# Kernel optimization log

Measured on AMD Instinct MI355X. Metric: run time of the kernel, lower is better.

The kernel has to match this reference:

```python
import jax, jax.numpy as jnp
from jax import lax
import numpy as np

B, L, IN_DIM, HID, BINS = 1, 384, 41, 64, 63
ATTN_DIM, NUM_ANCHORS = 32, 32
NUM_CONV, ATTN_EVERY = 6, 2
SIGMA, EPS = 12.0, 1e-5
DILATIONS = [1, 2, 4, 8, 16]


def select_anchors(length, k):
    # deterministic 'stride' mode of select_anchors
    k = max(1, min(k, length))
    stride = max(1, length // k)
    idx = np.arange(0, length, stride)[:k]
    if idx.size < k:
        idx = np.concatenate([idx, np.full(k - idx.size, length - 1)])
    return jnp.asarray(idx, dtype=jnp.int32)


def conv2d(x, w, b, dilation=1):
    # x: (b, Cin, H, W), w: (Cout, Cin, kh, kw) -- 'same' padding like torch padding=dilation*(k//2)
    pad = dilation * (w.shape[-1] // 2)
    y = lax.conv_general_dilated(x, w, (1, 1), [(pad, pad), (pad, pad)],
                                 rhs_dilation=(dilation, dilation),
                                 dimension_numbers=('NCHW', 'OIHW', 'NCHW'))
    return y + b[None, :, None, None]


def instance_norm(x):
    # torch InstanceNorm2d(affine=False), eps=1e-5, per (b, c) over spatial dims
    mu = x.mean(axis=(2, 3), keepdims=True)
    var = x.var(axis=(2, 3), keepdims=True)
    return (x - mu) * lax.rsqrt(var + EPS)


def anchor_attention(pair, td, tq, anchors, wq, wl, wr, wvl, wvr, wo, wg, bg,
                     tg_w1, tg_b1, tg_w2, tg_b2):
    # pair: (b, L, L, d); td: (b, L, L); tq: (b,)
    q = pair @ wq                                    # (b, L, L, a)
    p_left = pair[:, :, anchors, :]                  # (b, L, K, d)
    p_right = pair[:, anchors, :, :]                 # (b, K, L, d)
    left = p_left @ wl                               # (b, L, K, a)
    right = p_right @ wr                             # (b, K, L, a)
    scores = jnp.einsum('bija,bika->bijk', q, left)
    scores = scores + jnp.einsum('bija,bkja->bijk', q, right)
    scores = scores / jnp.sqrt(jnp.float32(ATTN_DIM))
    # template bias, 'consistency' mode
    t_left = td[:, :, anchors]                       # (b, L, K)
    t_right = jnp.swapaxes(td[:, anchors, :], 1, 2)  # (b, L, K)
    t_sum = t_left[:, :, None, :] + t_right[:, None, :, :]  # (b, L, L, K)
    bias = -jnp.abs(t_sum - td[..., None]) / SIGMA
    # TemplateGate
    coverage = (td > 0).astype(jnp.float32).mean(axis=(1, 2))        # (b,)
    length_norm = jnp.full_like(coverage, td.shape[-1] / 512.0)
    feats = jnp.stack([coverage, tq, length_norm], axis=-1)          # (b, 3)
    g = jax.nn.sigmoid(jax.nn.relu(feats @ tg_w1 + tg_b1) @ tg_w2 + tg_b2)  # (b, 1)
    scores = scores + g[:, :, None, None] * bias
    attn = jax.nn.softmax(scores, axis=-1)
    v_left = p_left @ wvl                            # (b, L, K, a)
    v_right = p_right @ wvr                          # (b, K, L, a)
    update = jnp.einsum('bijk,bika->bija', attn, v_left)
    update = update + jnp.einsum('bijk,bkja->bija', attn, v_right)
    update = update @ wo                             # (b, L, L, d)
    gate = jax.nn.sigmoid(pair @ wg + bg)
    return pair + gate * update


def setup_inputs() -> dict:
    key = jax.random.key(0)
    ks = iter(jax.random.split(key, 40))

    def rn(shape, scale=0.05):
        return jax.random.normal(next(ks), shape, dtype=jnp.float32) * scale

    return dict(
        features=jax.random.normal(next(ks), (B, L, L, IN_DIM), dtype=jnp.float32),
        template_dist=jax.random.uniform(next(ks), (B, L, L), dtype=jnp.float32) * 20.0,
        template_quality=jax.random.uniform(next(ks), (B,), dtype=jnp.float32),
        in_w=rn((HID, IN_DIM, 1, 1)), in_b=rn((HID,)),
        conv1_w=rn((NUM_CONV, HID, HID, 3, 3)), conv1_b=rn((NUM_CONV, HID)),
        conv2_w=rn((NUM_CONV, HID, HID, 3, 3)), conv2_b=rn((NUM_CONV, HID)),
        wq=rn((HID, ATTN_DIM)), wl=rn((HID, ATTN_DIM)), wr=rn((HID, ATTN_DIM)),
        wvl=rn((HID, ATTN_DIM)), wvr=rn((HID, ATTN_DIM)), wo=rn((ATTN_DIM, HID)),
        wg=rn((HID, HID)), bg=rn((HID,)),
        tg_w1=rn((3, 16)), tg_b1=rn((16,)), tg_w2=rn((16, 1)), tg_b2=rn((1,)),
        dist_w=rn((BINS, HID, 3, 3)), dist_b=rn((BINS,)),
        cf_w1=rn((32, BINS, 3, 3)), cf_b1=rn((32,)),
        cf_w2=rn((32, 32, 3, 3)), cf_b2=rn((32,)),
        cf_w3=rn((1, 32, 1, 1)), cf_b3=rn((1,)),
    )


def reference(features, template_dist, template_quality, in_w, in_b,
              conv1_w, conv1_b, conv2_w, conv2_b,
              wq, wl, wr, wvl, wvr, wo, wg, bg, tg_w1, tg_b1, tg_w2, tg_b2,
              dist_w, dist_b, cf_w1, cf_b1, cf_w2, cf_b2, cf_w3, cf_b3):
    anchors = select_anchors(L, NUM_ANCHORS)
    x = conv2d(jnp.transpose(features, (0, 3, 1, 2)), in_w, in_b)  # (b, hid, L, L)
    num_attn = max(1, NUM_CONV // max(1, ATTN_EVERY))
    attn_added = 0
    for i in range(NUM_CONV):
        d = DILATIONS[i % len(DILATIONS)]
        res = x
        out = jax.nn.elu(instance_norm(conv2d(x, conv1_w[i], conv1_b[i], d)))
        out = instance_norm(conv2d(out, conv2_w[i], conv2_b[i], 1))
        x = jax.nn.elu(out + res)
        if (i + 1) % ATTN_EVERY == 0 and attn_added < num_attn:
            pair = jnp.transpose(x, (0, 2, 3, 1))
            pair = anchor_attention(pair, template_dist, template_quality, anchors,
                                    wq, wl, wr, wvl, wvr, wo, wg, bg,
                                    tg_w1, tg_b1, tg_w2, tg_b2)
            x = jnp.transpose(pair, (0, 3, 1, 2))
            attn_added += 1
    logits = conv2d(x, dist_w, dist_b)                       # (b, bins, L, L)
    logits = 0.5 * (logits + jnp.swapaxes(logits, 2, 3))     # symmetrize_pairs
    c = jax.nn.relu(conv2d(logits, cf_w1, cf_b1))
    c = jax.nn.relu(conv2d(c, cf_w2, cf_b2))
    confidence = jax.nn.sigmoid(conv2d(c, cf_w3, cf_b3))[:, 0]   # (b, L, L)
    distance_logits = jnp.transpose(logits, (0, 2, 3, 1))        # (b, L, L, bins)
    return distance_logits, confidence
```

## Files before the change

kernel.cpp:

```cpp
#include <hip/hip_runtime.h>
#include <math.h>

#define LDIM 384
#define NPIX (LDIM*LDIM)
#define NBINS 63

typedef __attribute__((ext_vector_type(8))) __bf16 bf16x8;
typedef __attribute__((ext_vector_type(4))) float floatx4;

__device__ __forceinline__ float sigf(float x){ return 1.f/(1.f+expf(-x)); }

__global__ __launch_bounds__(256) void prep_kernel(
    const float* __restrict__ c1w, const float* __restrict__ c2w,
    const float* __restrict__ dw, const float* __restrict__ cf1w,
    const float* __restrict__ cf2w, const float* __restrict__ wg,
    const float* __restrict__ wo, const float* __restrict__ wq,
    __bf16* __restrict__ Wf){
  int idx = blockIdx.x*256 + threadIdx.x;
  if (idx >= 515072) return;
  if (idx >= 506880){
    int rel, NT, NDIM; const float* src;
    if (idx < 510976){ rel = idx - 506880; src = wg; NT=4; NDIM=64; }
    else if (idx < 513024){ rel = idx - 510976; src = wo; NT=4; NDIM=64; }
    else { rel = idx - 513024; src = wq; NT=2; NDIM=32; }
    int j = rel & 7, lane = (rel>>3) & 63;
    int r2 = rel >> 9;
    int nt = r2 % NT, kc = r2 / NT;
    int k = kc*32 + (lane>>4)*8 + j;
    int n = nt*16 + (lane&15);
    Wf[idx] = (__bf16)src[(size_t)k*NDIM + n];
    return;
  }
  const float* src; int ICreal, OCreal, ICP, NT, rel;
  if (idx < 442368){
    int layer = idx / 36864; rel = idx - layer*36864;
    int i = layer >> 1;
    src = (layer & 1) ? (c2w + (size_t)i*36864) : (c1w + (size_t)i*36864);
    ICreal=64; OCreal=64; ICP=64; NT=4;
  } else if (idx < 479232){
    rel = idx - 442368; src = dw;   ICreal=64; OCreal=63; ICP=64; NT=4;
  } else if (idx < 497664){
    rel = idx - 479232; src = cf1w; ICreal=63; OCreal=32; ICP=64; NT=2;
  } else {
    rel = idx - 497664; src = cf2w; ICreal=32; OCreal=32; ICP=32; NT=2;
  }
  int j = rel & 7, lane = (rel>>3) & 63;
  int r2 = rel >> 9;
  int nt = r2 % NT; int r3 = r2 / NT;
  int KC = ICP/32;
  int kc = r3 % KC; int tap = r3 / KC;
  int k = kc*32 + (lane>>4)*8 + j;
  int n = nt*16 + (lane&15);
  float v = 0.f;
  if (k < ICreal && n < OCreal) v = src[((size_t)n*ICreal + k)*9 + tap];
  Wf[idx] = (__bf16)v;
}

template<int ICP, int NT, int D, int WAVES>
__global__ __launch_bounds__(WAVES*64) void mfma_conv(
    const __bf16* __restrict__ Ain, const __bf16* __restrict__ Wf,
    const float* __restrict__ bias, int OC_real,
    float* __restrict__ outF, __bf16* __restrict__ outP,
    int relu, float* __restrict__ ostats){
  constexpr int KC = ICP/32;
  constexpr int OCS = NT*16;
  constexpr int REC_B = ICP*4;
  __shared__ float red[OCS*WAVES*2];
  const int t = threadIdx.x;
  const int wave = t>>6, lane = t&63;
  const int q = lane>>4, col16 = lane&15;
  const int y = blockIdx.y;
  const int x0 = blockIdx.x*(WAVES*16);
  const int gx0 = x0 + wave*16 + col16;

  floatx4 acc[NT];
  #pragma unroll
  for (int b=0;b<NT;b++){ floatx4 z = {0.f,0.f,0.f,0.f}; acc[b]=z; }

  #pragma unroll
  for (int ky=0; ky<3; ky++){
    const int yr = y + (ky-1)*D;
    if ((unsigned)yr < LDIM){
      const char* rowb = (const char*)Ain + (size_t)yr*LDIM*REC_B + q*16;
      #pragma unroll
      for (int kx=0; kx<3; kx++){
        const int gx = gx0 + (kx-1)*D;
        bf16x8 ah[KC], al[KC];
        #pragma unroll
        for (int kc=0;kc<KC;kc++){
          #pragma unroll
          for (int j=0;j<8;j++){ ah[kc][j]=(__bf16)0.f; al[kc][j]=(__bf16)0.f; }
        }
        if ((unsigned)gx < LDIM){
          const char* p = rowb + (size_t)gx*REC_B;
          #pragma unroll
          for (int kc=0;kc<KC;kc++){
            ah[kc] = *(const bf16x8*)(p + kc*64);
            al[kc] = *(const bf16x8*)(p + kc*64 + ICP*2);
          }
        }
        #pragma unroll
        for (int kc=0;kc<KC;kc++){
          const __bf16* wkc = Wf + (size_t)((ky*3+kx)*KC + kc)*NT*512 + lane*8;
          #pragma unroll
          for (int nt=0; nt<NT; nt++){
            bf16x8 bfrag = *(const bf16x8*)(wkc + (size_t)nt*512);
            acc[nt] = __builtin_amdgcn_mfma_f32_16x16x32_bf16(ah[kc], bfrag, acc[nt], 0,0,0);
            acc[nt] = __builtin_amdgcn_mfma_f32_16x16x32_bf16(al[kc], bfrag, acc[nt], 0,0,0);
          }
        }
      }
    }
  }

  #pragma unroll
  for (int nt=0; nt<NT; nt++){
    int oc = nt*16 + col16;
    float bv = (oc < OC_real) ? bias[oc] : 0.f;
    int pxb = x0 + wave*16 + q*4;
    float s=0.f, sq=0.f;
    #pragma unroll
    for (int r=0; r<4; r++){
      float vv = acc[nt][r] + bv;
      if (relu) vv = fmaxf(vv, 0.f);
      size_t pix = (size_t)y*LDIM + pxb + r;
      if (outF) outF[pix*OCS + oc] = vv;
      if (outP){
        __bf16 h = (__bf16)vv;
        __bf16* rec = outP + pix*(size_t)(OCS*2);
        rec[oc] = h; rec[OCS+oc] = (__bf16)(vv - (float)h);
      }
      s += vv; sq += vv*vv;
    }
    if (ostats){
      s  += __shfl_xor(s, 16);  s  += __shfl_xor(s, 32);
      sq += __shfl_xor(sq, 16); sq += __shfl_xor(sq, 32);
      if (q == 0){
        red[oc*WAVES + wave] = s;
        red[OCS*WAVES + oc*WAVES + wave] = sq;
      }
    }
  }
  if (ostats){
    __syncthreads();
    float* oslot = ostats + ((blockIdx.y & 7) << 7);
    if (t < OCS){
      float s=0.f, sq=0.f;
      #pragma unroll
      for (int w=0; w<WAVES; w++){
        s  += red[t*WAVES + w];
        sq += red[OCS*WAVES + t*WAVES + w];
      }
      atomicAdd(&oslot[t], s);
      atomicAdd(&oslot[64+t], sq);
    }
  }
}

__global__ __launch_bounds__(256) void in_proj_kernel(
    const float* __restrict__ feat, const float* __restrict__ w,
    const float* __restrict__ b, __bf16* __restrict__ PX){
  __shared__ float sf[16][41];
  __shared__ float sw[64*41];
  int t = threadIdx.x;
  size_t p0 = (size_t)blockIdx.x*16;
  float wv[11];
  #pragma unroll
  for (int k=0;k<11;k++){ int idx=t+k*256; wv[k] = (idx<2624) ? w[idx] : 0.f; }
  float fv[3];
  #pragma unroll
  for (int k=0;k<3;k++){ int idx=t+k*256; fv[k] = (idx<656) ? feat[p0*41 + idx] : 0.f; }
  #pragma unroll
  for (int k=0;k<11;k++){ int idx=t+k*256; if (idx<2624) sw[idx]=wv[k]; }
  #pragma unroll
  for (int k=0;k<3;k++){
    int idx=t+k*256;
    if (idx<656){ int p = idx/41, k2 = idx - p*41; sf[p][k2]=fv[k]; }
  }
  __syncthreads();
  #pragma unroll
  for (int k=0;k<4;k++){
    int item = t + k*256;
    int c = item&63, p = item>>6;
    float acc = b[c];
    #pragma unroll
    for (int kk=0;kk<41;kk++) acc += sf[p][kk]*sw[c*41+kk];
    __bf16 h = (__bf16)acc;
    __bf16* rec = PX + (p0+p)*128;
    rec[c] = h; rec[64+c] = (__bf16)(acc - (float)h);
  }
}

__global__ __launch_bounds__(256) void norm_elu_planes(
    __bf16* __restrict__ U, const float* __restrict__ stats){
  size_t idx = (size_t)blockIdx.x*256 + threadIdx.x;
  size_t px = idx>>3; int c0 = (int)(idx&7)*8;
  __bf16* ur = U + px*128;
  uint4 uh = *(const uint4*)(ur + c0);
  uint4 ul = *(const uint4*)(ur + 64 + c0);
  __bf16* uhp=(__bf16*)&uh; __bf16* ulp=(__bf16*)&ul;
  float mu[8], rs[8];
  #pragma unroll
  for (int k=0;k<8;k++){
    int c = c0+k;
    float s=0.f, sq=0.f;
    #pragma unroll
    for (int rp=0;rp<8;rp++){ s += stats[rp*128 + c]; sq += stats[rp*128 + 64 + c]; }
    float m = s*(1.f/NPIX);
    mu[k]=m; rs[k]=rsqrtf(sq*(1.f/NPIX) - m*m + 1e-5f);
  }
  #pragma unroll
  for (int k=0;k<8;k++){
    float v = ((float)uhp[k] + (float)ulp[k] - mu[k])*rs[k];
    v = v>0.f ? v : expm1f(v);
    __bf16 h = (__bf16)v; uhp[k]=h; ulp[k]=(__bf16)(v-(float)h);
  }
  *(uint4*)(ur + c0) = uh;
  *(uint4*)(ur + 64 + c0) = ul;
}

__global__ __launch_bounds__(256) void norm_res_elu_planes(
    const __bf16* __restrict__ U, __bf16* __restrict__ PX,
    const float* __restrict__ stats){
  size_t idx = (size_t)blockIdx.x*256 + threadIdx.x;
  size_t px = idx>>3; int c0 = (int)(idx&7)*8;
  const __bf16* ur = U + px*128;
  __bf16* xr = PX + px*128;
  uint4 uh = *(const uint4*)(ur + c0);
  uint4 ul = *(const uint4*)(ur + 64 + c0);
  uint4 xh = *(uint4*)(xr + c0);
  uint4 xl = *(uint4*)(xr + 64 + c0);
  __bf16* uhp=(__bf16*)&uh; __bf16* ulp=(__bf16*)&ul;
  __bf16* xhp=(__bf16*)&xh; __bf16* xlp=(__bf16*)&xl;
  float mu[8], rs[8];
  #pragma unroll
  for (int k=0;k<8;k++){
    int c = c0+k;
    float s=0.f, sq=0.f;
    #pragma unroll
    for (int rp=0;rp<8;rp++){ s += stats[rp*128 + c]; sq += stats[rp*128 + 64 + c]; }
    float m = s*(1.f/NPIX);
    mu[k]=m; rs[k]=rsqrtf(sq*(1.f/NPIX) - m*m + 1e-5f);
  }
  #pragma unroll
  for (int k=0;k<8;k++){
    float v = ((float)uhp[k] + (float)ulp[k] - mu[k])*rs[k]
            + ((float)xhp[k] + (float)xlp[k]);
    v = v>0.f ? v : expm1f(v);
    __bf16 h = (__bf16)v; xhp[k]=h; xlp[k]=(__bf16)(v-(float)h);
  }
  *(uint4*)(xr + c0) = xh;
  *(uint4*)(xr + 64 + c0) = xl;
}

__global__ __launch_bounds__(256) void g_partial_kernel(
    const float* __restrict__ td, float* __restrict__ GC){
  size_t base = (size_t)blockIdx.x*256;
  float cnt = (td[base + threadIdx.x] > 0.f) ? 1.f : 0.f;
  __shared__ float red[256];
  red[threadIdx.x]=cnt; __syncthreads();
  for (int st=128; st; st>>=1){
    if (threadIdx.x<st) red[threadIdx.x]+=red[threadIdx.x+st];
    __syncthreads();
  }
  if (threadIdx.x==0) atomicAdd(GC, red[0]);
}

__global__ void g_final_kernel(
    const float* __restrict__ GC, const float* __restrict__ tq,
    const float* __restrict__ w1, const float* __restrict__ b1,
    const float* __restrict__ w2, const float* __restrict__ b2,
    float* __restrict__ G){
  if (threadIdx.x==0){
    float f0 = GC[0]*(1.f/NPIX), f1 = tq[0], f2 = (float)LDIM/512.f;
    float z = b2[0];
    for (int j=0;j<16;j++){
      float h = f0*w1[j] + f1*w1[16+j] + f2*w1[32+j] + b1[j];
      z += (h>0.f?h:0.f)*w2[j];
    }
    G[0] = sigf(z);
  }
}

__global__ __launch_bounds__(256) void qproj_mfma_kernel(
    const __bf16* __restrict__ PX, const __bf16* __restrict__ WqF,
    __bf16* __restrict__ Qb){
  const int t=threadIdx.x, wave=t>>6, lane=t&63, q=lane>>4, col16=lane&15;
  const size_t p0=(size_t)blockIdx.x*128;
  __shared__ __bf16 Xhi[128*72];
  __shared__ __bf16 Xlo[128*72];
  uint4 sv[8];
  #pragma unroll
  for (int k=0;k<8;k++){
    int c=t+k*256;
    sv[k] = *(const uint4*)((const char*)PX + (p0 + (c>>4))*256 + (c&15)*16);
  }
  #pragma unroll
  for (int k=0;k<8;k++){
    int c=t+k*256; int px=c>>4, sub=c&15;
    *(uint4*)(((sub<8)?Xhi:Xlo) + px*72 + (sub&7)*8) = sv[k];
  }
  __syncthreads();
  floatx4 acc[2][2];
  #pragma unroll
  for (int a=0;a<2;a++)
    #pragma unroll
    for (int b=0;b<2;b++){ floatx4 z={0.f,0.f,0.f,0.f}; acc[a][b]=z; }
  #pragma unroll
  for (int kc=0;kc<2;kc++){
    bf16x8 ah[2], al[2];
    #pragma unroll
    for (int mt=0;mt<2;mt++){
      int row = wave*32 + mt*16 + col16;
      ah[mt] = *(const bf16x8*)(Xhi + row*72 + kc*32 + q*8);
      al[mt] = *(const bf16x8*)(Xlo + row*72 + kc*32 + q*8);
    }
    #pragma unroll
    for (int nt=0;nt<2;nt++){
      bf16x8 b = *(const bf16x8*)(WqF + (kc*2+nt)*512 + lane*8);
      acc[0][nt] = __builtin_amdgcn_mfma_f32_16x16x32_bf16(ah[0], b, acc[0][nt], 0,0,0);
      acc[1][nt] = __builtin_amdgcn_mfma_f32_16x16x32_bf16(ah[1], b, acc[1][nt], 0,0,0);
      acc[0][nt] = __builtin_amdgcn_mfma_f32_16x16x32_bf16(al[0], b, acc[0][nt], 0,0,0);
      acc[1][nt] = __builtin_amdgcn_mfma_f32_16x16x32_bf16(al[1], b, acc[1][nt], 0,0,0);
    }
  }
  #pragma unroll
  for (int mt=0;mt<2;mt++){
    size_t pxb = p0 + wave*32 + mt*16 + q*4;
    #pragma unroll
    for (int nt=0;nt<2;nt++){
      int oc = nt*16 + col16;
      #pragma unroll
      for (int r=0;r<4;r++)
        Qb[(pxb+r)*32 + oc] = (__bf16)acc[mt][nt][r];
    }
  }
}

__global__ __launch_bounds__(256) void proj_left_kernel(
    const __bf16* __restrict__ PX, const float* __restrict__ wl, const float* __restrict__ wvl,
    __bf16* __restrict__ leftb, __bf16* __restrict__ vleftTb){
  int i = blockIdx.x;
  __shared__ float xa[32][65];
  __shared__ float w1s[2048], w2s[2048];
  int c = threadIdx.x & 63;
  for (int a = threadIdx.x>>6; a<32; a+=4){
    const __bf16* rec = PX + ((size_t)i*LDIM + 12*a)*128;
    xa[a][c] = (float)rec[c] + (float)rec[64+c];
  }
  for (int idx=threadIdx.x; idx<2048; idx+=256){ w1s[idx]=wl[idx]; w2s[idx]=wvl[idx]; }
  __syncthreads();
  #pragma unroll
  for (int k=0;k<4;k++){
    int idx = threadIdx.x + k*256;
    int a = idx>>5, n = idx&31;
    float a1=0.f, a2=0.f;
    #pragma unroll
    for (int cc=0;cc<64;cc++){ float v=xa[a][cc]; a1+=v*w1s[cc*32+n]; a2+=v*w2s[cc*32+n]; }
    leftb  [(size_t)i*1024 + a*32 + n] = (__bf16)a1;
    vleftTb[(size_t)i*1024 + n*32 + a] = (__bf16)a2;
  }
}

__global__ __launch_bounds__(256) void proj_right_kernel(
    const __bf16* __restrict__ PX, const float* __restrict__ wr, const float* __restrict__ wvr,
    __bf16* __restrict__ rightb, __bf16* __restrict__ vrightTb){
  int a = blockIdx.y; int row = 12*a;
  int j0 = blockIdx.x*32;
  __shared__ float xr[32][65];
  __shared__ float w1s[2048], w2s[2048];
  for (int idx=threadIdx.x; idx<2048; idx+=256){ w1s[idx]=wr[idx]; w2s[idx]=wvr[idx]; }
  int c = threadIdx.x & 63;
  for (int jl = threadIdx.x>>6; jl<32; jl+=4){
    const __bf16* rec = PX + ((size_t)row*LDIM + j0 + jl)*128;
    xr[jl][c] = (float)rec[c] + (float)rec[64+c];
  }
  __syncthreads();
  #pragma unroll
  for (int k=0;k<4;k++){
    int idx=threadIdx.x+k*256; int jl=idx>>5, n=idx&31;
    float a1=0.f, a2=0.f;
    #pragma unroll
    for (int cc=0;cc<64;cc++){ float v=xr[jl][cc]; a1+=v*w1s[cc*32+n]; a2+=v*w2s[cc*32+n]; }
    rightb  [(size_t)(j0+jl)*1024 + a*32 + n] = (__bf16)a1;
    vrightTb[(size_t)(j0+jl)*1024 + n*32 + a] = (__bf16)a2;
  }
}

__global__ __launch_bounds__(256) void attn_s1_kernel(
    const __bf16* __restrict__ Qb, const __bf16* __restrict__ leftb,
    float* __restrict__ S){
  const int t=threadIdx.x, wave=t>>6, lane=t&63, q=lane>>4, col16=lane&15;
  const int i = blockIdx.y, j0 = blockIdx.x*128;
  bf16x8 bfrag[2];
  #pragma unroll
  for (int nt=0;nt<2;nt++)
    bfrag[nt] = *(const bf16x8*)(leftb + (size_t)i*1024 + (nt*16+col16)*32 + q*8);
  bf16x8 ah[2];
  #pragma unroll
  for (int mt=0;mt<2;mt++){
    int row = j0 + wave*32 + mt*16 + col16;
    ah[mt] = *(const bf16x8*)(Qb + ((size_t)i*LDIM + row)*32 + q*8);
  }
  floatx4 acc[2][2];
  #pragma unroll
  for (int a=0;a<2;a++)
    #pragma unroll
    for (int b=0;b<2;b++){ floatx4 z={0.f,0.f,0.f,0.f}; acc[a][b]=z; }
  #pragma unroll
  for (int mt=0;mt<2;mt++)
    #pragma unroll
    for (int nt=0;nt<2;nt++)
      acc[mt][nt] = __builtin_amdgcn_mfma_f32_16x16x32_bf16(ah[mt], bfrag[nt], acc[mt][nt], 0,0,0);
  #pragma unroll
  for (int mt=0;mt<2;mt++){
    int jb = j0 + wave*32 + mt*16 + q*4;
    #pragma unroll
    for (int nt=0;nt<2;nt++){
      int a = nt*16 + col16;
      #pragma unroll
      for (int r=0;r<4;r++)
        S[((size_t)i*LDIM + jb + r)*32 + a] = acc[mt][nt][r];
    }
  }
}

__global__ __launch_bounds__(256) void attn_s2_kernel(
    const __bf16* __restrict__ Qb, const __bf16* __restrict__ rightb,
    float* __restrict__ S){
  const int t=threadIdx.x, wave=t>>6, lane=t&63, q=lane>>4, col16=lane&15;
  const int j = blockIdx.y, i0 = blockIdx.x*128;
  bf16x8 bfrag[2];
  #pragma unroll
  for (int nt=0;nt<2;nt++)
    bfrag[nt] = *(const bf16x8*)(rightb + (size_t)j*1024 + (nt*16+col16)*32 + q*8);
  bf16x8 ah[2];
  #pragma unroll
  for (int mt=0;mt<2;mt++){
    int row = i0 + wave*32 + mt*16 + col16;
    ah[mt] = *(const bf16x8*)(Qb + ((size_t)row*LDIM + j)*32 + q*8);
  }
  floatx4 acc[2][2];
  #pragma unroll
  for (int a=0;a<2;a++)
    #pragma unroll
    for (int b=0;b<2;b++){ floatx4 z={0.f,0.f,0.f,0.f}; acc[a][b]=z; }
  #pragma unroll
  for (int mt=0;mt<2;mt++)
    #pragma unroll
    for (int nt=0;nt<2;nt++)
      acc[mt][nt] = __builtin_amdgcn_mfma_f32_16x16x32_bf16(ah[mt], bfrag[nt], acc[mt][nt], 0,0,0);
  #pragma unroll
  for (int mt=0;mt<2;mt++){
    int ib = i0 + wave*32 + mt*16 + q*4;
    #pragma unroll
    for (int nt=0;nt<2;nt++){
      int a = nt*16 + col16;
      #pragma unroll
      for (int r=0;r<4;r++){
        size_t idx = ((size_t)(ib+r)*LDIM + j)*32 + a;
        S[idx] += acc[mt][nt][r];
      }
    }
  }
}

__global__ __launch_bounds__(128) void attn_soft_kernel(
    const float* __restrict__ S, const float* __restrict__ td,
    const float* __restrict__ gp, __bf16* __restrict__ attnb,
    __bf16* __restrict__ attnTb){
  int i = blockIdx.y;
  int j0 = blockIdx.x*128;
  int t = threadIdx.x;
  int j = j0 + t;
  __shared__ float tl[32];
  __shared__ float trS[32*128];
  {
    #pragma unroll
    for (int v=0; v<8; v++){
      int f = t + v*128;
      int a = f>>5, jl4 = (f&31)*4;
      *(floatx4*)(trS + a*128 + jl4) = *(const floatx4*)(td + (size_t)(12*a)*LDIM + j0 + jl4);
    }
    if (t<32) tl[t] = td[(size_t)i*LDIM + 12*t];
  }
  __syncthreads();
  float g = gp[0];
  float tdij = td[(size_t)i*LDIM+j];
  float s[32];
  const floatx4* sp4 = (const floatx4*)(S + ((size_t)i*LDIM+j)*32);
  #pragma unroll
  for (int v=0;v<8;v++){
    floatx4 sv = sp4[v];
    #pragma unroll
    for (int e=0;e<4;e++) s[v*4+e] = sv[e];
  }
  float m = -1e30f;
  #pragma unroll
  for (int a=0;a<32;a++){
    float acc = s[a]*0.17677669529663687f;
    float bias = -fabsf(tl[a] + trS[a*128 + t] - tdij) * (1.0f/12.0f);
    acc += g*bias;
    s[a]=acc;
    m = fmaxf(m, acc);
  }
  float sum=0.f;
  #pragma unroll
  for (int a=0;a<32;a++){ s[a]=expf(s[a]-m); sum+=s[a]; }
  float inv = 1.f/sum;
  bf16x8 pk[4];
  #pragma unroll
  for (int v=0;v<4;v++){
    #pragma unroll
    for (int e=0;e<8;e++) pk[v][e] = (__bf16)(s[v*8+e]*inv);
  }
  bf16x8* op = (bf16x8*)(attnb + ((size_t)i*LDIM+j)*32);
  bf16x8* opT = (bf16x8*)(attnTb + ((size_t)j*LDIM+i)*32);
  #pragma unroll
  for (int v=0;v<4;v++){ op[v]=pk[v]; opT[v]=pk[v]; }
}

__global__ __launch_bounds__(256) void attn_u1_kernel(
    const __bf16* __restrict__ attnb, const __bf16* __restrict__ vleftTb,
    float* __restrict__ UPD){
  const int t=threadIdx.x, wave=t>>6, lane=t&63, q=lane>>4, col16=lane&15;
  const int i = blockIdx.y, j0 = blockIdx.x*128;
  bf16x8 bfrag[2];
  #pragma unroll
  for (int nt=0;nt<2;nt++)
    bfrag[nt] = *(const bf16x8*)(vleftTb + (size_t)i*1024 + (nt*16+col16)*32 + q*8);
  bf16x8 ah[2];
  #pragma unroll
  for (int mt=0;mt<2;mt++){
    int row = j0 + wave*32 + mt*16 + col16;
    ah[mt] = *(const bf16x8*)(attnb + ((size_t)i*LDIM + row)*32 + q*8);
  }
  floatx4 acc[2][2];
  #pragma unroll
  for (int a=0;a<2;a++)
    #pragma unroll
    for (int b=0;b<2;b++){ floatx4 z={0.f,0.f,0.f,0.f}; acc[a][b]=z; }
  #pragma unroll
  for (int mt=0;mt<2;mt++)
    #pragma unroll
    for (int nt=0;nt<2;nt++)
      acc[mt][nt] = __builtin_amdgcn_mfma_f32_16x16x32_bf16(ah[mt], bfrag[nt], acc[mt][nt], 0,0,0);
  #pragma unroll
  for (int mt=0;mt<2;mt++){
    int jb = j0 + wave*32 + mt*16 + q*4;
    #pragma unroll
    for (int nt=0;nt<2;nt++){
      int c = nt*16 + col16;
      #pragma unroll
      for (int r=0;r<4;r++)
        UPD[((size_t)i*LDIM + jb + r)*32 + c] = acc[mt][nt][r];
    }
  }
}

__global__ __launch_bounds__(256) void attn_u2_kernel(
    const __bf16* __restrict__ attnTb, const __bf16* __restrict__ vrightTb,
    float* __restrict__ UPD){
  const int t=threadIdx.x, wave=t>>6, lane=t&63, q=lane>>4, col16=lane&15;
  const int j = blockIdx.y, i0 = blockIdx.x*128;
  bf16x8 bfrag[2];
  #pragma unroll
  for (int nt=0;nt<2;nt++)
    bfrag[nt] = *(const bf16x8*)(vrightTb + (size_t)j*1024 + (nt*16+col16)*32 + q*8);
  bf16x8 ah[2];
  #pragma unroll
  for (int mt=0;mt<2;mt++){
    int row = i0 + wave*32 + mt*16 + col16;
    ah[mt] = *(const bf16x8*)(attnTb + ((size_t)j*LDIM + row)*32 + q*8);
  }
  floatx4 acc[2][2];
  #pragma unroll
  for (int a=0;a<2;a++)
    #pragma unroll
    for (int b=0;b<2;b++){ floatx4 z={0.f,0.f,0.f,0.f}; acc[a][b]=z; }
  #pragma unroll
  for (int mt=0;mt<2;mt++)
    #pragma unroll
    for (int nt=0;nt<2;nt++)
      acc[mt][nt] = __builtin_amdgcn_mfma_f32_16x16x32_bf16(ah[mt], bfrag[nt], acc[mt][nt], 0,0,0);
  #pragma unroll
  for (int mt=0;mt<2;mt++){
    int ib = i0 + wave*32 + mt*16 + q*4;
    #pragma unroll
    for (int nt=0;nt<2;nt++){
      int c = nt*16 + col16;
      #pragma unroll
      for (int r=0;r<4;r++){
        size_t idx = ((size_t)(ib+r)*LDIM + j)*32 + c;
        UPD[idx] += acc[mt][nt][r];
      }
    }
  }
}

__global__ __launch_bounds__(256) void gate_mfma_kernel(
    __bf16* __restrict__ PX, const float* __restrict__ UPD,
    const __bf16* __restrict__ WgF, const __bf16* __restrict__ WoF,
    const float* __restrict__ bg){
  const int t=threadIdx.x, wave=t>>6, lane=t&63, q=lane>>4, col16=lane&15;
  const size_t p0=(size_t)blockIdx.x*128;
  __shared__ __bf16 Xhi[128*72];
  __shared__ __bf16 Xlo[128*72];
  __shared__ __bf16 Ub[128*40];
  uint4 sv[8];
  #pragma unroll
  for (int k=0;k<8;k++){
    int c=t+k*256;
    sv[k] = *(const uint4*)((const char*)PX + (p0 + (c>>4))*256 + (c&15)*16);
  }
  floatx4 uv[4];
  #pragma unroll
  for (int k=0;k<4;k++){
    int p = (t>>3) + k*32;
    uv[k] = *(const floatx4*)(UPD + (p0+p)*32 + (t&7)*4);
  }
  #pragma unroll
  for (int k=0;k<8;k++){
    int c=t+k*256; int px=c>>4, sub=c&15;
    *(uint4*)(((sub<8)?Xhi:Xlo) + px*72 + (sub&7)*8) = sv[k];
  }
  #pragma unroll
  for (int k=0;k<4;k++){
    int p = (t>>3) + k*32;
    __bf16* pu = Ub + p*40 + (t&7)*4;
    #pragma unroll
    for (int kk=0;kk<4;kk++) pu[kk]=(__bf16)uv[k][kk];
  }
  __syncthreads();
  floatx4 accg[2][4], accu[2][4];
  #pragma unroll
  for (int a=0;a<2;a++)
    #pragma unroll
    for (int b=0;b<4;b++){ floatx4 z={0.f,0.f,0.f,0.f}; accg[a][b]=z; accu[a][b]=z; }
  #pragma unroll
  for (int kc=0;kc<2;kc++){
    bf16x8 ah[2], al[2];
    #pragma unroll
    for (int mt=0;mt<2;mt++){
      int row = wave*32 + mt*16 + col16;
      ah[mt] = *(const bf16x8*)(Xhi + row*72 + kc*32 + q*8);
      al[mt] = *(const bf16x8*)(Xlo + row*72 + kc*32 + q*8);
    }
    #pragma unroll
    for (int nt=0;nt<4;nt++){
      bf16x8 b = *(const bf16x8*)(WgF + (kc*4+nt)*512 + lane*8);
      accg[0][nt] = __builtin_amdgcn_mfma_f32_16x16x32_bf16(ah[0], b, accg[0][nt], 0,0,0);
      accg[1][nt] = __builtin_amdgcn_mfma_f32_16x16x32_bf16(ah[1], b, accg[1][nt], 0,0,0);
      accg[0][nt] = __builtin_amdgcn_mfma_f32_16x16x32_bf16(al[0], b, accg[0][nt], 0,0,0);
      accg[1][nt] = __builtin_amdgcn_mfma_f32_16x16x32_bf16(al[1], b, accg[1][nt], 0,0,0);
    }
  }
  {
    bf16x8 au[2];
    #pragma unroll
    for (int mt=0;mt<2;mt++){
      int row = wave*32 + mt*16 + col16;
      au[mt] = *(const bf16x8*)(Ub + row*40 + q*8);
    }
    #pragma unroll
    for (int nt=0;nt<4;nt++){
      bf16x8 b = *(const bf16x8*)(WoF + nt*512 + lane*8);
      accu[0][nt] = __builtin_amdgcn_mfma_f32_16x16x32_bf16(au[0], b, accu[0][nt], 0,0,0);
      accu[1][nt] = __builtin_amdgcn_mfma_f32_16x16x32_bf16(au[1], b, accu[1][nt], 0,0,0);
    }
  }
  #pragma unroll
  for (int mt=0;mt<2;mt++){
    size_t pxb = p0 + wave*32 + mt*16 + q*4;
    #pragma unroll
    for (int nt=0;nt<4;nt++){
      int oc = nt*16 + col16;
      float bgv = bg[oc];
      #pragma unroll
      for (int r=0;r<4;r++){
        __bf16* rec = PX + (pxb+r)*128;
        float xv = (float)rec[oc] + (float)rec[64+oc];
        float g = sigf(accg[mt][nt][r] + bgv);
        float xn = xv + g*accu[mt][nt][r];
        __bf16 h = (__bf16)xn;
        rec[oc] = h; rec[64+oc] = (__bf16)(xn - (float)h);
      }
    }
  }
}

__global__ __launch_bounds__(256) void sym_kernel(
    const float* __restrict__ lg, __bf16* __restrict__ PS, float* __restrict__ dout){
  int i = blockIdx.y;
  int j = blockIdx.x*4 + (threadIdx.x>>6);
  int o = threadIdx.x & 63;
  float v = 0.5f*(lg[((size_t)i*LDIM+j)*64+o] + lg[((size_t)j*LDIM+i)*64+o]);
  size_t pix = (size_t)i*LDIM+j;
  __bf16 h = (__bf16)v;
  __bf16* rec = PS + pix*128;
  rec[o] = h; rec[64+o] = (__bf16)(v - (float)h);
  if (o<63) dout[pix*63+o] = v;
}

__global__ __launch_bounds__(256) void conf_kernel(
    const float* __restrict__ c2, const float* __restrict__ w,
    const float* __restrict__ b, float* __restrict__ out){
  int t = threadIdx.x;
  size_t pix = (size_t)blockIdx.x*8 + (t>>5);
  int c = t&31;
  float v = c2[pix*32 + c]*w[c];
  #pragma unroll
  for (int off=16; off; off>>=1) v += __shfl_xor(v, off);
  if (c==0) out[pix] = sigf(v + b[0]);
}

extern "C" void kernel_launch(void* const* d_in, const int* in_sizes, int n_in,
                              void* d_out, int out_size, void* d_ws, size_t ws_size,
                              hipStream_t stream){
  const float* feat = (const float*)d_in[0];
  const float* td   = (const float*)d_in[1];
  const float* tq   = (const float*)d_in[2];
  const float* in_w = (const float*)d_in[3];
  const float* in_b = (const float*)d_in[4];
  const float* c1w  = (const float*)d_in[5];
  const float* c1b  = (const float*)d_in[6];
  const float* c2w  = (const float*)d_in[7];
  const float* c2b  = (const float*)d_in[8];
  const float* wq   = (const float*)d_in[9];
  const float* wl   = (const float*)d_in[10];
  const float* wr   = (const float*)d_in[11];
  const float* wvl  = (const float*)d_in[12];
  const float* wvr  = (const float*)d_in[13];
  const float* wo   = (const float*)d_in[14];
  const float* wg   = (const float*)d_in[15];
  const float* bg   = (const float*)d_in[16];
  const float* tgw1 = (const float*)d_in[17];
  const float* tgb1 = (const float*)d_in[18];
  const float* tgw2 = (const float*)d_in[19];
  const float* tgb2 = (const float*)d_in[20];
  const float* dw   = (const float*)d_in[21];
  const float* db   = (const float*)d_in[22];
  const float* cf1w = (const float*)d_in[23];
  const float* cf1b = (const float*)d_in[24];
  const float* cf2w = (const float*)d_in[25];
  const float* cf2b = (const float*)d_in[26];
  const float* cf3w = (const float*)d_in[27];
  const float* cf3b = (const float*)d_in[28];

  float* ws = (float*)d_ws;
  const size_t BUF = (size_t)64*NPIX;
  float* R1 = ws;
  float* R2 = ws + BUF;
  float* R3 = ws + 2*BUF;
  float* STATS = ws + 3*BUF;
  float* G     = STATS + 12288;
  float* GC    = G + 1;
  __bf16* WF   = (__bf16*)(G + 16);
  __bf16* WGF  = WF + 506880;
  __bf16* WOF  = WF + 510976;
  __bf16* WQF  = WF + 513024;

  __bf16* PX = (__bf16*)R1;
  __bf16* PT = (__bf16*)R2;
  __bf16* PU = (__bf16*)R3;
  char* R2c = (char*)R2;
  __bf16* Qb       = (__bf16*)R2c;
  __bf16* ATTNB    = (__bf16*)(R2c +  9437184);
  __bf16* ATTNTB   = (__bf16*)(R2c + 18874368);
  __bf16* LEFTB    = (__bf16*)(R2c + 28311552);
  __bf16* RIGHTB   = (__bf16*)(R2c + 29097984);
  __bf16* VLEFTTB  = (__bf16*)(R2c + 29884416);
  __bf16* VRIGHTTB = (__bf16*)(R2c + 30670848);
  float* S   = R3;
  float* UPD = R3 + (size_t)32*NPIX;

  hipMemsetAsync(STATS, 0, (12288 + 16)*sizeof(float), stream);
  prep_kernel<<<2012, 256, 0, stream>>>(c1w, c2w, dw, cf1w, cf2w, wg, wo, wq, WF);
  g_partial_kernel<<<576, 256, 0, stream>>>(td, GC);
  g_final_kernel<<<1, 64, 0, stream>>>(GC, tq, tgw1, tgb1, tgw2, tgb2, G);

  in_proj_kernel<<<9216, 256, 0, stream>>>(feat, in_w, in_b, PX);

#define CONV2_NORM(i) \
  norm_elu_planes<<<4608, 256, 0, stream>>>(PT, STATS + (2*(i))*1024); \
  mfma_conv<64,4,1,4><<<dim3(6,LDIM), 256, 0, stream>>>( \
      PT, WF + (size_t)(2*(i)+1)*36864, c2b + (i)*64, 64, \
      nullptr, PU, 0, STATS + (2*(i)+1)*1024); \
  norm_res_elu_planes<<<4608, 256, 0, stream>>>(PU, PX, STATS + (2*(i)+1)*1024);

#define CONV1(i, DD) \
  mfma_conv<64,4,DD,4><<<dim3(6,LDIM), 256, 0, stream>>>( \
      PX, WF + (size_t)(2*(i))*36864, c1b + (i)*64, 64, \
      nullptr, PT, 0, STATS + (2*(i))*1024);

#define ATTN_BLOCK \
  qproj_mfma_kernel<<<1152, 256, 0, stream>>>(PX, WQF, Qb); \
  proj_left_kernel<<<384, 256, 0, stream>>>(PX, wl, wvl, LEFTB, VLEFTTB); \
  proj_right_kernel<<<dim3(12,32), 256, 0, stream>>>(PX, wr, wvr, RIGHTB, VRIGHTTB); \
  attn_s1_kernel<<<dim3(3,LDIM), 256, 0, stream>>>(Qb, LEFTB, S); \
  attn_s2_kernel<<<dim3(3,LDIM), 256, 0, stream>>>(Qb, RIGHTB, S); \
  attn_soft_kernel<<<dim3(3,LDIM), 128, 0, stream>>>(S, td, G, ATTNB, ATTNTB); \
  attn_u1_kernel<<<dim3(3,LDIM), 256, 0, stream>>>(ATTNB, VLEFTTB, UPD); \
  attn_u2_kernel<<<dim3(3,LDIM), 256, 0, stream>>>(ATTNTB, VRIGHTTB, UPD); \
  gate_mfma_kernel<<<1152, 256, 0, stream>>>(PX, UPD, WGF, WOF, bg);

  CONV1(0, 1)   CONV2_NORM(0)
  CONV1(1, 2)   CONV2_NORM(1)  ATTN_BLOCK
  CONV1(2, 4)   CONV2_NORM(2)
  CONV1(3, 8)   CONV2_NORM(3)  ATTN_BLOCK
  CONV1(4, 16)  CONV2_NORM(4)
  CONV1(5, 1)   CONV2_NORM(5)  ATTN_BLOCK

  mfma_conv<64,4,1,4><<<dim3(6,LDIM), 256, 0, stream>>>(
      PX, WF + 442368, db, 63, R3, nullptr, 0, nullptr);
  sym_kernel<<<dim3(96,LDIM), 256, 0, stream>>>(R3, PT, (float*)d_out);
  mfma_conv<64,2,1,4><<<dim3(6,LDIM), 256, 0, stream>>>(
      PT, WF + 479232, cf1b, 32, nullptr, PX, 1, nullptr);
  mfma_conv<32,2,1,4><<<dim3(6,LDIM), 256, 0, stream>>>(
      PX, WF + 497664, cf2b, 32, R3, nullptr, 1, nullptr);
  conf_kernel<<<18432, 256, 0, stream>>>(R3, cf3w, cf3b, (float*)d_out + (size_t)NPIX*NBINS);
}
```

Before: 1.750 ms.

## Stage conv input rows into LDS with async double-buffered global_load_lds

The MFMA 3x3 conv now stages each input row strip (with halo) into shared memory using global_load_lds, double-buffering across the three kernel rows so the next row's load overlaps MFMA work on the current one. Shared-memory reads use an XOR swizzle to avoid bank conflicts, and out-of-bounds halo pixels are zeroed in LDS. Previously every lane issued redundant direct global loads for each of the 9 taps. The cost is dynamic shared memory sized per dilation, which may limit occupancy for large dilations, plus extra barriers and hand-written waitcnt sequencing.

```diff
diff --git a/kernel.cpp b/kernel.cpp
--- a/kernel.cpp
+++ b/kernel.cpp
@@ -56,6 +56,10 @@
   Wf[idx] = (__bf16)v;
 }
 
+#define VMCNT(N) asm volatile("s_waitcnt vmcnt(%0)" :: "n"(N) : "memory")
+#define LGKM0()  asm volatile("s_waitcnt lgkmcnt(0)" ::: "memory")
+#define BARS()   { __builtin_amdgcn_s_barrier(); __builtin_amdgcn_sched_barrier(0); }
+
 template<int ICP, int NT, int D, int WAVES>
 __global__ __launch_bounds__(WAVES*64) void mfma_conv(
     const __bf16* __restrict__ Ain, const __bf16* __restrict__ Wf,
@@ -65,60 +69,115 @@
   constexpr int KC = ICP/32;
   constexpr int OCS = NT*16;
   constexpr int REC_B = ICP*4;
-  __shared__ float red[OCS*WAVES*2];
+  constexpr int PPX = REC_B/16;
+  constexpr int HALF = PPX/2;
+  constexpr int W = WAVES*16;
+  constexpr int T = WAVES*64;
+  constexpr int SW = W + 2*D;
+  constexpr int TOT1 = SW*PPX;
+  constexpr int NITER = (TOT1 + T - 1)/T;
+  constexpr int BUFB = NITER*T*16;
+  extern __shared__ __align__(16) char smem[];
+  char* buf0 = smem;
+  char* buf1 = smem + BUFB;
   const int t = threadIdx.x;
   const int wave = t>>6, lane = t&63;
   const int q = lane>>4, col16 = lane&15;
   const int y = blockIdx.y;
-  const int x0 = blockIdx.x*(WAVES*16);
-  const int gx0 = x0 + wave*16 + col16;
+  const int x0 = blockIdx.x*W;
+
+  int srcoff[NITER];
+  bool oob[NITER];
+  #pragma unroll
+  for (int k=0;k<NITER;k++){
+    int s = k*T + t;
+    int px = s / PPX;
+    int sub = s % PPX;
+    int cg = sub ^ (px & 7);
+    int gx = x0 - D + px;
+    oob[k] = (px < SW) && ((unsigned)gx >= LDIM);
+    int gxc = min(max(gx,0), LDIM-1);
+    srcoff[k] = gxc*REC_B + cg*16;
+  }
+
+  auto STAGE = [&](char* buf, int ky){
+    int yr = y + (ky-1)*D;
+    int yc = min(max(yr,0), LDIM-1);
+    const char* rb = (const char*)Ain + (size_t)yc*LDIM*REC_B;
+    #pragma unroll
+    for (int k=0;k<NITER;k++){
+      char* ldsb = buf + ((size_t)k*T + wave*64)*16;
+      const char* src = rb + srcoff[k];
+      __builtin_amdgcn_global_load_lds(
+          (const __attribute__((address_space(1))) void*)src,
+          (__attribute__((address_space(3))) void*)ldsb, 16, 0, 0);
+    }
+  };
+  auto ZOOB = [&](char* buf){
+    #pragma unroll
+    for (int k=0;k<NITER;k++)
+      if (oob[k]){ uint4 z={0u,0u,0u,0u}; *(uint4*)(buf + ((size_t)k*T + t)*16) = z; }
+  };
 
   floatx4 acc[NT];
   #pragma unroll
   for (int b=0;b<NT;b++){ floatx4 z = {0.f,0.f,0.f,0.f}; acc[b]=z; }
 
-  #pragma unroll
-  for (int ky=0; ky<3; ky++){
-    const int yr = y + (ky-1)*D;
-    if ((unsigned)yr < LDIM){
-      const char* rowb = (const char*)Ain + (size_t)yr*LDIM*REC_B + q*16;
+  auto MFMA_PHASE = [&](const char* buf, int ky){
+    int yr = y + (ky-1)*D;
+    if ((unsigned)yr >= LDIM) return;
+    #pragma unroll
+    for (int kx=0;kx<3;kx++){
+      int cl = wave*16 + col16 + kx*D;
+      int e = cl & 7;
+      bf16x8 wf[KC][NT];
       #pragma unroll
-      for (int kx=0; kx<3; kx++){
-        const int gx = gx0 + (kx-1)*D;
-        bf16x8 ah[KC], al[KC];
+      for (int kc=0;kc<KC;kc++){
+        const __bf16* wkc = Wf + (size_t)((ky*3+kx)*KC + kc)*NT*512 + lane*8;
         #pragma unroll
-        for (int kc=0;kc<KC;kc++){
-          #pragma unroll
-          for (int j=0;j<8;j++){ ah[kc][j]=(__bf16)0.f; al[kc][j]=(__bf16)0.f; }
-        }
-        if ((unsigned)gx < LDIM){
-          const char* p = rowb + (size_t)gx*REC_B;
-          #pragma unroll
-          for (int kc=0;kc<KC;kc++){
-            ah[kc] = *(const bf16x8*)(p + kc*64);
-            al[kc] = *(const bf16x8*)(p + kc*64 + ICP*2);
-          }
-        }
+        for (int nt=0;nt<NT;nt++)
+          wf[kc][nt] = *(const bf16x8*)(wkc + (size_t)nt*512);
+      }
+      #pragma unroll
+      for (int kc=0;kc<KC;kc++){
+        int sh = (kc*4+q) ^ e;
+        int sl = (HALF + kc*4+q) ^ e;
+        bf16x8 ah = *(const bf16x8*)(buf + (size_t)cl*REC_B + sh*16);
+        bf16x8 al = *(const bf16x8*)(buf + (size_t)cl*REC_B + sl*16);
         #pragma unroll
-        for (int kc=0;kc<KC;kc++){
-          const __bf16* wkc = Wf + (size_t)((ky*3+kx)*KC + kc)*NT*512 + lane*8;
-          #pragma unroll
-          for (int nt=0; nt<NT; nt++){
-            bf16x8 bfrag = *(const bf16x8*)(wkc + (size_t)nt*512);
-            acc[nt] = __builtin_amdgcn_mfma_f32_16x16x32_bf16(ah[kc], bfrag, acc[nt], 0,0,0);
-            acc[nt] = __builtin_amdgcn_mfma_f32_16x16x32_bf16(al[kc], bfrag, acc[nt], 0,0,0);
-          }
+        for (int nt=0;nt<NT;nt++){
+          acc[nt] = __builtin_amdgcn_mfma_f32_16x16x32_bf16(ah, wf[kc][nt], acc[nt], 0,0,0);
+          acc[nt] = __builtin_amdgcn_mfma_f32_16x16x32_bf16(al, wf[kc][nt], acc[nt], 0,0,0);
         }
       }
     }
-  }
-
+  };
+
+  STAGE(buf0, 0);
+  STAGE(buf1, 1);
+  VMCNT(NITER);
+  ZOOB(buf0); LGKM0();
+  BARS();
+  MFMA_PHASE(buf0, 0);
+  BARS();
+  STAGE(buf0, 2);
+  VMCNT(NITER);
+  ZOOB(buf1); LGKM0();
+  BARS();
+  MFMA_PHASE(buf1, 1);
+  VMCNT(0);
+  ZOOB(buf0); LGKM0();
+  BARS();
+  MFMA_PHASE(buf0, 2);
+
+  float sAcc[NT], sqAcc[NT];
+  #pragma unroll
+  for (int nt=0;nt<NT;nt++){ sAcc[nt]=0.f; sqAcc[nt]=0.f; }
   #pragma unroll
   for (int nt=0; nt<NT; nt++){
     int oc = nt*16 + col16;
     float bv = (oc < OC_real) ? bias[oc] : 0.f;
     int pxb = x0 + wave*16 + q*4;
-    float s=0.f, sq=0.f;
     #pragma unroll
     for (int r=0; r<4; r++){
       float vv = acc[nt][r] + bv;
@@ -130,9 +189,16 @@
         __bf16* rec = outP + pix*(size_t)(OCS*2);
         rec[oc] = h; rec[OCS+oc] = (__bf16)(vv - (float)h);
       }
-      s += vv; sq += vv*vv;
-    }
-    if (ostats){
+      sAcc[nt] += vv; sqAcc[nt] += vv*vv;
+    }
+  }
+  if (ostats){
+    float* red = (float*)smem;
+    __syncthreads();
+    #pragma unroll
+    for (int nt=0; nt<NT; nt++){
+      int oc = nt*16 + col16;
+      float s = sAcc[nt], sq = sqAcc[nt];
       s  += __shfl_xor(s, 16);  s  += __shfl_xor(s, 32);
       sq += __shfl_xor(sq, 16); sq += __shfl_xor(sq, 32);
       if (q == 0){
@@ -140,8 +206,6 @@
         red[OCS*WAVES + oc*WAVES + wave] = sq;
       }
     }
-  }
-  if (ostats){
     __syncthreads();
     float* oslot = ostats + ((blockIdx.y & 7) << 7);
     if (t < OCS){
@@ -781,15 +845,18 @@
 
   in_proj_kernel<<<9216, 256, 0, stream>>>(feat, in_w, in_b, PX);
 
+#define CONV_SMEM(ICP_, DD, WW) \
+  (2 * (((((WW)*16+2*(DD))*((ICP_)/4)) + ((WW)*64) - 1)/((WW)*64)) * ((WW)*64) * 16)
+
 #define CONV2_NORM(i) \
   norm_elu_planes<<<4608, 256, 0, stream>>>(PT, STATS + (2*(i))*1024); \
-  mfma_conv<64,4,1,4><<<dim3(6,LDIM), 256, 0, stream>>>( \
+  mfma_conv<64,4,1,4><<<dim3(6,LDIM), 256, CONV_SMEM(64,1,4), stream>>>( \
       PT, WF + (size_t)(2*(i)+1)*36864, c2b + (i)*64, 64, \
       nullptr, PU, 0, STATS + (2*(i)+1)*1024); \
   norm_res_elu_planes<<<4608, 256, 0, stream>>>(PU, PX, STATS + (2*(i)+1)*1024);
 
 #define CONV1(i, DD) \
-  mfma_conv<64,4,DD,4><<<dim3(6,LDIM), 256, 0, stream>>>( \
+  mfma_conv<64,4,DD,4><<<dim3(6,LDIM), 256, CONV_SMEM(64,DD,4), stream>>>( \
       PX, WF + (size_t)(2*(i))*36864, c1b + (i)*64, 64, \
       nullptr, PT, 0, STATS + (2*(i))*1024);
 
@@ -811,12 +878,12 @@
   CONV1(4, 16)  CONV2_NORM(4)
   CONV1(5, 1)   CONV2_NORM(5)  ATTN_BLOCK
 
-  mfma_conv<64,4,1,4><<<dim3(6,LDIM), 256, 0, stream>>>(
+  mfma_conv<64,4,1,4><<<dim3(6,LDIM), 256, CONV_SMEM(64,1,4), stream>>>(
       PX, WF + 442368, db, 63, R3, nullptr, 0, nullptr);
   sym_kernel<<<dim3(96,LDIM), 256, 0, stream>>>(R3, PT, (float*)d_out);
-  mfma_conv<64,2,1,4><<<dim3(6,LDIM), 256, 0, stream>>>(
+  mfma_conv<64,2,1,4><<<dim3(6,LDIM), 256, CONV_SMEM(64,1,4), stream>>>(
       PT, WF + 479232, cf1b, 32, nullptr, PX, 1, nullptr);
-  mfma_conv<32,2,1,4><<<dim3(6,LDIM), 256, 0, stream>>>(
+  mfma_conv<32,2,1,4><<<dim3(6,LDIM), 256, CONV_SMEM(32,1,4), stream>>>(
       PX, WF + 497664, cf2b, 32, R3, nullptr, 1, nullptr);
   conf_kernel<<<18432, 256, 0, stream>>>(R3, cf3w, cf3b, (float*)d_out + (size_t)NPIX*NBINS);
 }
```

Measured after the change: 1.477 ms. 15.6% less time.
